# Performance work log

Measured on AMD Instinct MI355X. Metric: run time of the kernel, lower is better.

## Reference

```python
import jax, jax.numpy as jnp
import numpy as np

HQ, HK, D = 16, 4, 64
WINDOW = 1024  # sliding-window left size; right=0 (causal)
GATE_CH = 12
RMS_EPS = 1e-8


def rms_norm(x):
    return x * jax.lax.rsqrt(jnp.mean(x * x, axis=-1, keepdims=True) + RMS_EPS)


def apply_rope(x, cos, sin):
    # x: [B,T,H,D]; cos/sin: [T,D//2] broadcast to [1,T,1,D//2]
    x1, x2 = jnp.split(x, 2, axis=-1)
    c = cos[None, :, None, :]
    s = sin[None, :, None, :]
    return jnp.concatenate([x1 * c - x2 * s, x1 * s + x2 * c], axis=-1)


def setup_inputs() -> dict:
    key = jax.random.key(0)
    ks = jax.random.split(key, 7)
    B, T, E = 2, 2048, HQ * D
    x = jax.random.normal(ks[0], (B, T, E), jnp.float32)
    value_embeds = jax.random.normal(ks[1], (B, T, HK * D), jnp.float32)
    # rope cache: angles for half the head dim
    inv_freq = 1.0 / (10000.0 ** (jnp.arange(D // 2, dtype=jnp.float32) / (D // 2)))
    ang = jnp.arange(T, dtype=jnp.float32)[:, None] * inv_freq[None, :]
    rope_cos = jnp.cos(ang)
    rope_sin = jnp.sin(ang)
    std = (3.0 ** 0.5) * (E ** -0.5)
    w_qkv = jax.random.uniform(ks[2], ((HQ + 2 * HK) * D, E), jnp.float32, -std, std)
    w_gate = jax.random.normal(ks[3], (HK, GATE_CH), jnp.float32) * 0.02
    w_o = jax.random.normal(ks[4], (E, E), jnp.float32) * 0.02
    return {"x": x, "value_embeds": value_embeds, "rope_cos": rope_cos,
            "rope_sin": rope_sin, "w_qkv": w_qkv, "w_gate": w_gate, "w_o": w_o}


def reference(x, value_embeds, rope_cos, rope_sin, w_qkv, w_gate, w_o):
    B, T, E = x.shape
    groups = HQ // HK
    qkv = jnp.einsum('bte,fe->btf', x, w_qkv).reshape(B, T, HQ + 2 * HK, D)
    q = qkv[:, :, :HQ, :]
    k = qkv[:, :, HQ:HQ + HK, :]
    v = qkv[:, :, HQ + HK:, :]
    # value-embedding gating
    ve = value_embeds.reshape(B, T, HK, D)
    gate = 3.0 * jax.nn.sigmoid(jnp.einsum('btc,hc->bth', x[..., :GATE_CH], w_gate))
    v = v + gate[..., None] * ve
    # rope + qk-norm
    q = rms_norm(apply_rope(q, rope_cos, rope_sin))
    k = rms_norm(apply_rope(k, rope_cos, rope_sin))
    # GQA: repeat kv heads
    k_rep = jnp.repeat(k, groups, axis=2)  # [B,T,HQ,D]
    v_rep = jnp.repeat(v, groups, axis=2)
    scale = 1.0 / jnp.sqrt(jnp.float32(D))
    scores = jnp.einsum('bqhd,bkhd->bhqk', q, k_rep) * scale
    i = jnp.arange(T)[:, None]
    j = jnp.arange(T)[None, :]
    mask = (j <= i) & (j >= i - WINDOW)  # causal + sliding window
    scores = jnp.where(mask[None, None], scores, jnp.float32(-1e30))
    attn = jax.nn.softmax(scores, axis=-1)
    out = jnp.einsum('bhqk,bkhd->bqhd', attn, v_rep).reshape(B, T, E)
    out = jnp.einsum('bte,fe->btf', out, w_o)
    return out
```

## Files before the change

kernel.cpp:

```cpp
#include <hip/hip_runtime.h>
#include <math.h>

#define T_LEN 2048
#define NB 2
#define E_DIM 1024
#define F_DIM 1536
#define HQn 16
#define HKn 4
#define Dh 64
#define WIN 1024
#define GATE_CH 12
#define PS 72
#define PSV 68
#define CS 73

typedef unsigned short u16;
typedef unsigned int u32;
typedef __attribute__((ext_vector_type(8))) short bf16x8;
typedef __attribute__((ext_vector_type(4))) short bf16x4;
typedef __attribute__((ext_vector_type(4))) float f32x4;

#if __has_builtin(__builtin_amdgcn_mfma_f32_16x16x16bf16_1k)
#define MFMA16(A, B, C) __builtin_amdgcn_mfma_f32_16x16x16bf16_1k(A, B, C, 0, 0, 0)
#elif __has_builtin(__builtin_amdgcn_mfma_f32_16x16x16_bf16)
#define MFMA16(A, B, C) __builtin_amdgcn_mfma_f32_16x16x16_bf16(A, B, C, 0, 0, 0)
#else
static __device__ __forceinline__ f32x4 mfma16_asm(bf16x4 a, bf16x4 b, f32x4 c) {
  f32x4 d;
  asm volatile("s_nop 1\n\tv_mfma_f32_16x16x16_bf16 %0, %1, %2, %3\n\ts_nop 7\n\ts_nop 7"
               : "=v"(d) : "v"(a), "v"(b), "v"(c));
  return d;
}
#define MFMA16(A, B, C) mfma16_asm(A, B, C)
#endif

__device__ __forceinline__ u16 f2bf(float f) {
  union { float f; unsigned int u; } v; v.f = f;
  unsigned int u = v.u + 0x7FFF + ((v.u >> 16) & 1);
  return (u16)(u >> 16);
}
__device__ __forceinline__ float bf2f(u16 h) {
  union { unsigned int u; float f; } v; v.u = ((unsigned int)h) << 16;
  return v.f;
}
__device__ __forceinline__ u32 pack_bf2(float hi, float lo) {
  union { float f; u32 u; } a, b; a.f = hi; b.f = lo;
  return __builtin_amdgcn_perm(a.u + 0x8000u, b.u + 0x8000u, 0x07060302u);
}
__device__ __forceinline__ void async_copy16(const void* g, void* l) {
  __builtin_amdgcn_global_load_lds(
      (const __attribute__((address_space(1))) unsigned int*)g,
      (__attribute__((address_space(3))) unsigned int*)l, 16, 0, 0);
}

__global__ __launch_bounds__(256) void cvt_all(
    const float4* __restrict__ x, const float4* __restrict__ wqkv,
    const float4* __restrict__ wo, uint2* __restrict__ xb,
    uint2* __restrict__ wqb, uint2* __restrict__ wob)
{
  int blk = blockIdx.x;
  const float4* in; uint2* out; int i;
  if (blk < 4096)       { in = x;    out = xb;  i = blk * 256 + threadIdx.x; }
  else if (blk < 5632)  { in = wqkv; out = wqb; i = (blk - 4096) * 256 + threadIdx.x; }
  else                  { in = wo;   out = wob; i = (blk - 5632) * 256 + threadIdx.x; }
  float4 v = in[i];
  uint2 o;
  o.x = (unsigned)f2bf(v.x) | ((unsigned)f2bf(v.y) << 16);
  o.y = (unsigned)f2bf(v.z) | ((unsigned)f2bf(v.w) << 16);
  out[i] = o;
}

__global__ __launch_bounds__(256) void gemm_qkv(
    const u16* __restrict__ A, const u16* __restrict__ B,
    const float* __restrict__ x, const float* __restrict__ ve,
    const float* __restrict__ rcos, const float* __restrict__ rsin,
    const float* __restrict__ wg,
    u16* __restrict__ qa, u16* __restrict__ ka, u16* __restrict__ vt)
{
  constexpr int K = E_DIM;
  __shared__ u16 smem[8192];
  __shared__ float gateL[64];
  u16* As = smem;
  u16* Bs = smem + 4096;
  u16* Ct = smem;
  const int tid = threadIdx.x;
  const int wave = tid >> 6, lane = tid & 63;
  const int quad = lane >> 4, lanelow = lane & 15;
  const int row0 = blockIdx.x * 64;
  const int h    = blockIdx.y;
  const int col0 = h * 64;
  const int wm = (wave >> 1) * 32, wn = (wave & 1) * 32;

  f32x4 acc[2][2];
#pragma unroll
  for (int i = 0; i < 2; ++i)
#pragma unroll
    for (int j = 0; j < 2; ++j) acc[i][j] = (f32x4){0.f, 0.f, 0.f, 0.f};

  for (int k0 = 0; k0 < K; k0 += 64) {
    __syncthreads();
#pragma unroll
    for (int kk = 0; kk < 2; ++kk) {
      async_copy16(A + (size_t)(row0 + (tid >> 2)) * K + k0 + kk * 32 + (tid & 3) * 8,
                   &As[kk * 2048 + tid * 8]);
      async_copy16(B + (size_t)(col0 + (tid >> 2)) * K + k0 + kk * 32 + (tid & 3) * 8,
                   &Bs[kk * 2048 + tid * 8]);
    }
    __syncthreads();
#pragma unroll
    for (int kk = 0; kk < 2; ++kk) {
      bf16x8 a[2], b[2];
#pragma unroll
      for (int i = 0; i < 2; ++i)
        a[i] = *(const bf16x8*)&As[kk * 2048 + (wm + i * 16 + lanelow) * 32 + quad * 8];
#pragma unroll
      for (int j = 0; j < 2; ++j)
        b[j] = *(const bf16x8*)&Bs[kk * 2048 + (wn + j * 16 + lanelow) * 32 + quad * 8];
#pragma unroll
      for (int i = 0; i < 2; ++i)
#pragma unroll
        for (int j = 0; j < 2; ++j)
          acc[i][j] = __builtin_amdgcn_mfma_f32_16x16x32_bf16(a[i], b[j], acc[i][j], 0, 0, 0);
    }
  }

  __syncthreads();
#pragma unroll
  for (int i = 0; i < 2; ++i)
#pragma unroll
    for (int j = 0; j < 2; ++j)
#pragma unroll
      for (int reg = 0; reg < 4; ++reg) {
        int row = wm + i * 16 + quad * 4 + reg;
        int col = wn + j * 16 + lanelow;
        Ct[row * CS + col] = f2bf(acc[i][j][reg]);
      }
  __syncthreads();

  if (h < HQn + HKn) {
    const bool isq = (h < HQn);
    const int half = lane & 31;
    for (int t = wave * 16; t < wave * 16 + 16; ++t) {
      int tok = row0 + t;
      int tt = tok & (T_LEN - 1);
      float c = rcos[tt * 32 + half], s = rsin[tt * 32 + half];
      float x1 = bf2f(Ct[t * CS + half]);
      float x2 = bf2f(Ct[t * CS + half + 32]);
      float y = (lane < 32) ? (x1 * c - x2 * s) : (x1 * s + x2 * c);
      float ss = y * y;
#pragma unroll
      for (int o = 32; o; o >>= 1) ss += __shfl_xor(ss, o, 64);
      float v = y * rsqrtf(ss * (1.f / Dh) + 1e-8f);
      if (isq)
        qa[((size_t)tok * HQn + h) * Dh + lane] = f2bf(v * 0.1803368801f);
      else
        ka[((size_t)tok * HKn + (h - HQn)) * Dh + lane] = f2bf(v);
    }
  } else {
    const int hk = h - (HQn + HKn);
    if (tid < 64) {
      int tok = row0 + tid;
      float g = 0.f;
#pragma unroll
      for (int c = 0; c < GATE_CH; ++c)
        g += x[(size_t)tok * E_DIM + c] * wg[hk * GATE_CH + c];
      gateL[tid] = 3.f / (1.f + __expf(-g));
    }
    __syncthreads();
    for (int t = wave * 16; t < wave * 16 + 16; ++t) {
      int tok = row0 + t;
      float val = bf2f(Ct[t * CS + lane]) +
                  gateL[t] * ve[(size_t)tok * (HKn * Dh) + hk * Dh + lane];
      Ct[t * CS + lane] = f2bf(val);
    }
    __syncthreads();
    int d = tid >> 2, tseg = (tid & 3) * 16;
    int tokbase = row0 + tseg;
    int b = tokbase >> 11;
    int tloc = tokbase & (T_LEN - 1);
    u16 tmp[16];
#pragma unroll
    for (int e = 0; e < 16; ++e) tmp[e] = Ct[(tseg + e) * CS + d];
    u16* dst = vt + ((size_t)(b * HKn + hk) * Dh + d) * T_LEN + tloc;
#pragma unroll
    for (int p = 0; p < 2; ++p)
      *(uint4*)(dst + p * 8) = *(uint4*)&tmp[p * 8];
  }
}

template<int BM, int BN, int STORE_BF16>
__global__ __launch_bounds__(256) void gemm_async(
    const u16* __restrict__ A, const u16* __restrict__ B,
    void* __restrict__ Cv, int M, int N, int K)
{
  constexpr int MI = BM / 32, NJ = BN / 32;
  constexpr int NSA = BM / 64;
  constexpr int NSB = BN / 64;
  __shared__ u16 As[2][BM * 32];
  __shared__ u16 Bs[2][BN * 32];
  const int tid = threadIdx.x;
  const int wave = tid >> 6, lane = tid & 63;
  const int quad = lane >> 4, lanelow = lane & 15;
  const int row0 = blockIdx.x * BM;
  const int col0 = blockIdx.y * BN;
  const int wm = (wave >> 1) * (BM / 2), wn = (wave & 1) * (BN / 2);

  f32x4 acc[MI][NJ];
#pragma unroll
  for (int i = 0; i < MI; ++i)
#pragma unroll
    for (int j = 0; j < NJ; ++j) acc[i][j] = (f32x4){0.f, 0.f, 0.f, 0.f};

  for (int k0 = 0; k0 < K; k0 += 64) {
    __syncthreads();
#pragma unroll
    for (int kk = 0; kk < 2; ++kk) {
#pragma unroll
      for (int s = 0; s < NSA; ++s) {
        int slot = s * 256 + tid;
        async_copy16(A + (size_t)(row0 + (slot >> 2)) * K + k0 + kk * 32 + (slot & 3) * 8,
                     &As[kk][slot * 8]);
      }
#pragma unroll
      for (int s = 0; s < NSB; ++s) {
        int slot = s * 256 + tid;
        async_copy16(B + (size_t)(col0 + (slot >> 2)) * K + k0 + kk * 32 + (slot & 3) * 8,
                     &Bs[kk][slot * 8]);
      }
    }
    __syncthreads();
#pragma unroll
    for (int kk = 0; kk < 2; ++kk) {
      bf16x8 a[MI], b[NJ];
#pragma unroll
      for (int i = 0; i < MI; ++i)
        a[i] = *(const bf16x8*)&As[kk][(wm + i * 16 + lanelow) * 32 + quad * 8];
#pragma unroll
      for (int j = 0; j < NJ; ++j)
        b[j] = *(const bf16x8*)&Bs[kk][(wn + j * 16 + lanelow) * 32 + quad * 8];
#pragma unroll
      for (int i = 0; i < MI; ++i)
#pragma unroll
        for (int j = 0; j < NJ; ++j)
          acc[i][j] = __builtin_amdgcn_mfma_f32_16x16x32_bf16(a[i], b[j], acc[i][j], 0, 0, 0);
    }
  }

#pragma unroll
  for (int i = 0; i < MI; ++i)
#pragma unroll
    for (int j = 0; j < NJ; ++j) {
      int r = row0 + wm + i * 16 + quad * 4;
      int c = col0 + wn + j * 16 + lanelow;
#pragma unroll
      for (int reg = 0; reg < 4; ++reg) {
        if (STORE_BF16)
          ((u16*)Cv)[(size_t)(r + reg) * N + c] = f2bf(acc[i][j][reg]);
        else
          ((float*)Cv)[(size_t)(r + reg) * N + c] = acc[i][j][reg];
      }
    }
}

__global__ __launch_bounds__(256) void attn_mfma(
    const u16* __restrict__ qa, const u16* __restrict__ ka,
    const u16* __restrict__ vt_g, u16* __restrict__ att)
{
  __shared__ u16 Ks[2][64 * PS];
  __shared__ u16 Vt[2][64 * PSV];
  const int bx = blockIdx.x, h = blockIdx.y, b = blockIdx.z;
  const int j5 = bx & 7;
  const int t5 = (bx >> 3) & 3;
  const int tu = (t5 + (h >> 3) + 2 * b) & 3;
  const int qt = (tu == 0) ? j5
               : (tu == 1) ? (15 - j5)
                           : (16 + 2 * j5 + (tu & 1));
  const int hk = h >> 2;
  const int qb = qt * 64;
  const int tid = threadIdx.x;
  const int wave = tid >> 6, lane = tid & 63;
  const int quad = lane >> 4, lanelow = lane & 15;

  bf16x8 aQ[2];
#pragma unroll
  for (int kk = 0; kk < 2; ++kk)
    aQ[kk] = *(const bf16x8*)(qa +
        ((size_t)(b * T_LEN + qb + wave * 16 + lanelow) * HQn + h) * Dh +
        kk * 32 + quad * 8);

  f32x4 O[4];
  float l = 0.f;
#pragma unroll
  for (int dt = 0; dt < 4; ++dt) O[dt] = (f32x4){0.f, 0.f, 0.f, 0.f};

  const int kt0 = (qt >= 16) ? qt - 16 : 0;
  const int kt1 = qt;

  const int sr0 = tid >> 3,         sc0 = (tid & 7) * 8;
  const int sr1 = (tid + 256) >> 3, sc1 = ((tid + 256) & 7) * 8;
  const u16* kg = ka + (size_t)(b * T_LEN) * (HKn * Dh) + hk * Dh;
  const u16* vg = vt_g + (size_t)(b * HKn + hk) * Dh * T_LEN;

  {
    const int kb = kt0 * 64;
    uint4 k0 = *(const uint4*)(kg + (size_t)(kb + sr0) * (HKn * Dh) + sc0);
    uint4 k1 = *(const uint4*)(kg + (size_t)(kb + sr1) * (HKn * Dh) + sc1);
    uint4 v0 = *(const uint4*)(vg + (size_t)sr0 * T_LEN + kb + sc0);
    uint4 v1 = *(const uint4*)(vg + (size_t)sr1 * T_LEN + kb + sc1);
    *(uint4*)&Ks[0][sr0 * PS + sc0] = k0;
    *(uint4*)&Ks[0][sr1 * PS + sc1] = k1;
    *(uint2*)&Vt[0][sr0 * PSV + sc0]     = make_uint2(v0.x, v0.y);
    *(uint2*)&Vt[0][sr0 * PSV + sc0 + 4] = make_uint2(v0.z, v0.w);
    *(uint2*)&Vt[0][sr1 * PSV + sc1]     = make_uint2(v1.x, v1.y);
    *(uint2*)&Vt[0][sr1 * PSV + sc1 + 4] = make_uint2(v1.z, v1.w);
  }

  for (int kt = kt0; kt <= kt1; ++kt) {
    const int buf = (kt - kt0) & 1;
    const int kb = kt * 64;
    uint4 k0, k1, v0, v1;
    const bool more = (kt < kt1);
    if (more) {
      const int nb = kb + 64;
      k0 = *(const uint4*)(kg + (size_t)(nb + sr0) * (HKn * Dh) + sc0);
      k1 = *(const uint4*)(kg + (size_t)(nb + sr1) * (HKn * Dh) + sc1);
      v0 = *(const uint4*)(vg + (size_t)sr0 * T_LEN + nb + sc0);
      v1 = *(const uint4*)(vg + (size_t)sr1 * T_LEN + nb + sc1);
    }
    __syncthreads();

    f32x4 St[4];
#pragma unroll
    for (int jt = 0; jt < 4; ++jt) {
      bf16x8 aK0 = *(const bf16x8*)&Ks[buf][(jt * 16 + lanelow) * PS + quad * 8];
      bf16x8 aK1 = *(const bf16x8*)&Ks[buf][(jt * 16 + lanelow) * PS + 32 + quad * 8];
      f32x4 acc = (f32x4){-12.f, -12.f, -12.f, -12.f};
      acc = __builtin_amdgcn_mfma_f32_16x16x32_bf16(aK0, aQ[0], acc, 0, 0, 0);
      acc = __builtin_amdgcn_mfma_f32_16x16x32_bf16(aK1, aQ[1], acc, 0, 0, 0);
      St[jt] = acc;
    }
    if (kt == kt1) {
#pragma unroll
      for (int jt = 0; jt < 4; ++jt)
#pragma unroll
        for (int rr = 0; rr < 4; ++rr) {
          int ig = qb + wave * 16 + lanelow;
          int jg = kb + jt * 16 + quad * 4 + rr;
          if (jg > ig) St[jt][rr] = -1e30f;
        }
    } else if (kt == kt0 && qt >= 16) {
#pragma unroll
      for (int jt = 0; jt < 4; ++jt)
#pragma unroll
        for (int rr = 0; rr < 4; ++rr) {
          int ig = qb + wave * 16 + lanelow;
          int jg = kb + jt * 16 + quad * 4 + rr;
          if (jg < ig - WIN) St[jt][rr] = -1e30f;
        }
    }
    bf16x4 Pt[4];
#pragma unroll
    for (int jt = 0; jt < 4; ++jt) {
      float p0 = __builtin_amdgcn_exp2f(St[jt][0]);
      float p1 = __builtin_amdgcn_exp2f(St[jt][1]);
      float p2 = __builtin_amdgcn_exp2f(St[jt][2]);
      float p3 = __builtin_amdgcn_exp2f(St[jt][3]);
      l += (p0 + p1) + (p2 + p3);
      union { uint2 u; bf16x4 v; } pu;
      pu.u.x = pack_bf2(p1, p0);
      pu.u.y = pack_bf2(p3, p2);
      Pt[jt] = pu.v;
    }
#pragma unroll
    for (int dt = 0; dt < 4; ++dt)
#pragma unroll
      for (int jt = 0; jt < 4; ++jt) {
        bf16x4 aV = *(const bf16x4*)&Vt[buf][(dt * 16 + lanelow) * PSV + jt * 16 + quad * 4];
        O[dt] = MFMA16(aV, Pt[jt], O[dt]);
      }
    if (more) {
      const int nbuf = buf ^ 1;
      *(uint4*)&Ks[nbuf][sr0 * PS + sc0] = k0;
      *(uint4*)&Ks[nbuf][sr1 * PS + sc1] = k1;
      *(uint2*)&Vt[nbuf][sr0 * PSV + sc0]     = make_uint2(v0.x, v0.y);
      *(uint2*)&Vt[nbuf][sr0 * PSV + sc0 + 4] = make_uint2(v0.z, v0.w);
      *(uint2*)&Vt[nbuf][sr1 * PSV + sc1]     = make_uint2(v1.x, v1.y);
      *(uint2*)&Vt[nbuf][sr1 * PSV + sc1 + 4] = make_uint2(v1.z, v1.w);
    }
  }

  {
    float s = l;
    s += __shfl_xor(s, 16, 64);
    s += __shfl_xor(s, 32, 64);
    float inv = 1.f / s;
    int qg = qb + wave * 16 + lanelow;
    u16* obase = att + (size_t)(b * T_LEN + qg) * E_DIM + h * Dh;
#pragma unroll
    for (int dt = 0; dt < 4; ++dt) {
      bf16x4 ov;
      ov[0] = (short)f2bf(O[dt][0] * inv);
      ov[1] = (short)f2bf(O[dt][1] * inv);
      ov[2] = (short)f2bf(O[dt][2] * inv);
      ov[3] = (short)f2bf(O[dt][3] * inv);
      *(bf16x4*)(obase + dt * 16 + quad * 4) = ov;
    }
  }
}

extern "C" void kernel_launch(void* const* d_in, const int* in_sizes, int n_in,
                              void* d_out, int out_size, void* d_ws, size_t ws_size,
                              hipStream_t stream)
{
  const float* x    = (const float*)d_in[0];
  const float* ve   = (const float*)d_in[1];
  const float* rc   = (const float*)d_in[2];
  const float* rs   = (const float*)d_in[3];
  const float* wqkv = (const float*)d_in[4];
  const float* wg   = (const float*)d_in[5];
  const float* wo   = (const float*)d_in[6];
  float* out = (float*)d_out;

  char* ws = (char*)d_ws;
  u16* x_bf    = (u16*)(ws);
  u16* wqkv_bf = (u16*)(ws + 8388608);
  u16* wo_bf   = (u16*)(ws + 11534336);
  u16* q_att   = (u16*)(ws + 13631488);
  u16* k_att   = (u16*)(ws + 22020096);
  u16* v_t     = (u16*)(ws + 24117248);
  u16* att     = (u16*)(ws + 26214400);

  cvt_all<<<6656, 256, 0, stream>>>((const float4*)x, (const float4*)wqkv,
                                    (const float4*)wo, (uint2*)x_bf,
                                    (uint2*)wqkv_bf, (uint2*)wo_bf);
  gemm_qkv<<<dim3(64, 24), 256, 0, stream>>>(x_bf, wqkv_bf, x, ve, rc, rs, wg,
                                             q_att, k_att, v_t);
  attn_mfma<<<dim3(T_LEN / 64, HQn, NB), 256, 0, stream>>>(q_att, k_att, v_t, att);
  gemm_async<64, 64, 0><<<dim3(64, 16), 256, 0, stream>>>(
      att, wo_bf, out, 4096, E_DIM, E_DIM);
}
```

Measured before the change: 161.0 us.

## Double-buffer GEMM smem with XOR swizzle and enlarge M tiles to 128

Both GEMM kernels now keep two shared-memory buffers and prefetch the next K tile with async copies while the MFMAs run on the current one, so only one barrier per iteration remains. The shared tiles use a 64-wide row layout with an XOR swizzle to avoid LDS bank conflicts on the fragment reads. The QKV and output GEMMs grow from 64 to 128 rows per block, which improves operand reuse but halves the grid, so occupancy and wave count per CU drop. Shared memory use rises accordingly, and the QKV epilogue loops are resized for the larger tile.

```diff
diff --git a/kernel.cpp b/kernel.cpp
--- a/kernel.cpp
+++ b/kernel.cpp
@@ -78,55 +78,72 @@
     u16* __restrict__ qa, u16* __restrict__ ka, u16* __restrict__ vt)
 {
   constexpr int K = E_DIM;
-  __shared__ u16 smem[8192];
-  __shared__ float gateL[64];
+  __shared__ u16 smem[24576];
+  __shared__ float gateL[128];
   u16* As = smem;
-  u16* Bs = smem + 4096;
+  u16* Bs = smem + 16384;
   u16* Ct = smem;
   const int tid = threadIdx.x;
   const int wave = tid >> 6, lane = tid & 63;
   const int quad = lane >> 4, lanelow = lane & 15;
-  const int row0 = blockIdx.x * 64;
+  const int row0 = blockIdx.x * 128;
   const int h    = blockIdx.y;
   const int col0 = h * 64;
-  const int wm = (wave >> 1) * 32, wn = (wave & 1) * 32;
-
-  f32x4 acc[2][2];
-#pragma unroll
-  for (int i = 0; i < 2; ++i)
+  const int wm = (wave >> 1) * 64, wn = (wave & 1) * 32;
+
+  f32x4 acc[4][2];
+#pragma unroll
+  for (int i = 0; i < 4; ++i)
 #pragma unroll
     for (int j = 0; j < 2; ++j) acc[i][j] = (f32x4){0.f, 0.f, 0.f, 0.f};
 
+  auto stage = [&](int buf, int k0) {
+#pragma unroll
+    for (int s = 0; s < 4; ++s) {
+      int slot = s * 256 + tid;
+      int r = slot >> 3, g = (slot & 7) ^ (r & 7);
+      async_copy16(A + (size_t)(row0 + r) * K + k0 + g * 8,
+                   &As[buf * 8192 + slot * 8]);
+    }
+#pragma unroll
+    for (int s = 0; s < 2; ++s) {
+      int slot = s * 256 + tid;
+      int r = slot >> 3, g = (slot & 7) ^ (r & 7);
+      async_copy16(B + (size_t)(col0 + r) * K + k0 + g * 8,
+                   &Bs[buf * 4096 + slot * 8]);
+    }
+  };
+
+  stage(0, 0);
+  __syncthreads();
+  int cur = 0;
   for (int k0 = 0; k0 < K; k0 += 64) {
-    __syncthreads();
+    if (k0 + 64 < K) stage(cur ^ 1, k0 + 64);
 #pragma unroll
     for (int kk = 0; kk < 2; ++kk) {
-      async_copy16(A + (size_t)(row0 + (tid >> 2)) * K + k0 + kk * 32 + (tid & 3) * 8,
-                   &As[kk * 2048 + tid * 8]);
-      async_copy16(B + (size_t)(col0 + (tid >> 2)) * K + k0 + kk * 32 + (tid & 3) * 8,
-                   &Bs[kk * 2048 + tid * 8]);
-    }
-    __syncthreads();
-#pragma unroll
-    for (int kk = 0; kk < 2; ++kk) {
-      bf16x8 a[2], b[2];
-#pragma unroll
-      for (int i = 0; i < 2; ++i)
-        a[i] = *(const bf16x8*)&As[kk * 2048 + (wm + i * 16 + lanelow) * 32 + quad * 8];
-#pragma unroll
-      for (int j = 0; j < 2; ++j)
-        b[j] = *(const bf16x8*)&Bs[kk * 2048 + (wn + j * 16 + lanelow) * 32 + quad * 8];
-#pragma unroll
-      for (int i = 0; i < 2; ++i)
+      bf16x8 a[4], b[2];
+#pragma unroll
+      for (int i = 0; i < 4; ++i) {
+        int r = wm + i * 16 + lanelow;
+        a[i] = *(const bf16x8*)&As[cur * 8192 + r * 64 + (((kk * 4 + quad) ^ (r & 7)) * 8)];
+      }
+#pragma unroll
+      for (int j = 0; j < 2; ++j) {
+        int r = wn + j * 16 + lanelow;
+        b[j] = *(const bf16x8*)&Bs[cur * 4096 + r * 64 + (((kk * 4 + quad) ^ (r & 7)) * 8)];
+      }
+#pragma unroll
+      for (int i = 0; i < 4; ++i)
 #pragma unroll
         for (int j = 0; j < 2; ++j)
           acc[i][j] = __builtin_amdgcn_mfma_f32_16x16x32_bf16(a[i], b[j], acc[i][j], 0, 0, 0);
     }
-  }
-
-  __syncthreads();
-#pragma unroll
-  for (int i = 0; i < 2; ++i)
+    __syncthreads();
+    cur ^= 1;
+  }
+
+#pragma unroll
+  for (int i = 0; i < 4; ++i)
 #pragma unroll
     for (int j = 0; j < 2; ++j)
 #pragma unroll
@@ -140,7 +157,7 @@
   if (h < HQn + HKn) {
     const bool isq = (h < HQn);
     const int half = lane & 31;
-    for (int t = wave * 16; t < wave * 16 + 16; ++t) {
+    for (int t = wave * 32; t < wave * 32 + 32; ++t) {
       int tok = row0 + t;
       int tt = tok & (T_LEN - 1);
       float c = rcos[tt * 32 + half], s = rsin[tt * 32 + half];
@@ -158,7 +175,7 @@
     }
   } else {
     const int hk = h - (HQn + HKn);
-    if (tid < 64) {
+    if (tid < 128) {
       int tok = row0 + tid;
       float g = 0.f;
 #pragma unroll
@@ -167,23 +184,23 @@
       gateL[tid] = 3.f / (1.f + __expf(-g));
     }
     __syncthreads();
-    for (int t = wave * 16; t < wave * 16 + 16; ++t) {
+    for (int t = wave * 32; t < wave * 32 + 32; ++t) {
       int tok = row0 + t;
       float val = bf2f(Ct[t * CS + lane]) +
                   gateL[t] * ve[(size_t)tok * (HKn * Dh) + hk * Dh + lane];
       Ct[t * CS + lane] = f2bf(val);
     }
     __syncthreads();
-    int d = tid >> 2, tseg = (tid & 3) * 16;
+    int d = tid >> 2, tseg = (tid & 3) * 32;
     int tokbase = row0 + tseg;
     int b = tokbase >> 11;
     int tloc = tokbase & (T_LEN - 1);
-    u16 tmp[16];
-#pragma unroll
-    for (int e = 0; e < 16; ++e) tmp[e] = Ct[(tseg + e) * CS + d];
+    u16 tmp[32];
+#pragma unroll
+    for (int e = 0; e < 32; ++e) tmp[e] = Ct[(tseg + e) * CS + d];
     u16* dst = vt + ((size_t)(b * HKn + hk) * Dh + d) * T_LEN + tloc;
 #pragma unroll
-    for (int p = 0; p < 2; ++p)
+    for (int p = 0; p < 4; ++p)
       *(uint4*)(dst + p * 8) = *(uint4*)&tmp[p * 8];
   }
 }
@@ -194,10 +211,10 @@
     void* __restrict__ Cv, int M, int N, int K)
 {
   constexpr int MI = BM / 32, NJ = BN / 32;
-  constexpr int NSA = BM / 64;
-  constexpr int NSB = BN / 64;
-  __shared__ u16 As[2][BM * 32];
-  __shared__ u16 Bs[2][BN * 32];
+  constexpr int NSA = BM / 32;
+  constexpr int NSB = BN / 32;
+  __shared__ u16 As[2][BM * 64];
+  __shared__ u16 Bs[2][BN * 64];
   const int tid = threadIdx.x;
   const int wave = tid >> 6, lane = tid & 63;
   const int quad = lane >> 4, lanelow = lane & 15;
@@ -211,39 +228,47 @@
 #pragma unroll
     for (int j = 0; j < NJ; ++j) acc[i][j] = (f32x4){0.f, 0.f, 0.f, 0.f};
 
+  auto stage = [&](int buf, int k0) {
+#pragma unroll
+    for (int s = 0; s < NSA; ++s) {
+      int slot = s * 256 + tid;
+      int r = slot >> 3, g = (slot & 7) ^ (r & 7);
+      async_copy16(A + (size_t)(row0 + r) * K + k0 + g * 8, &As[buf][slot * 8]);
+    }
+#pragma unroll
+    for (int s = 0; s < NSB; ++s) {
+      int slot = s * 256 + tid;
+      int r = slot >> 3, g = (slot & 7) ^ (r & 7);
+      async_copy16(B + (size_t)(col0 + r) * K + k0 + g * 8, &Bs[buf][slot * 8]);
+    }
+  };
+
+  stage(0, 0);
+  __syncthreads();
+  int cur = 0;
   for (int k0 = 0; k0 < K; k0 += 64) {
-    __syncthreads();
-#pragma unroll
-    for (int kk = 0; kk < 2; ++kk) {
-#pragma unroll
-      for (int s = 0; s < NSA; ++s) {
-        int slot = s * 256 + tid;
-        async_copy16(A + (size_t)(row0 + (slot >> 2)) * K + k0 + kk * 32 + (slot & 3) * 8,
-                     &As[kk][slot * 8]);
-      }
-#pragma unroll
-      for (int s = 0; s < NSB; ++s) {
-        int slot = s * 256 + tid;
-        async_copy16(B + (size_t)(col0 + (slot >> 2)) * K + k0 + kk * 32 + (slot & 3) * 8,
-                     &Bs[kk][slot * 8]);
-      }
-    }
-    __syncthreads();
+    if (k0 + 64 < K) stage(cur ^ 1, k0 + 64);
 #pragma unroll
     for (int kk = 0; kk < 2; ++kk) {
       bf16x8 a[MI], b[NJ];
 #pragma unroll
-      for (int i = 0; i < MI; ++i)
-        a[i] = *(const bf16x8*)&As[kk][(wm + i * 16 + lanelow) * 32 + quad * 8];
-#pragma unroll
-      for (int j = 0; j < NJ; ++j)
-        b[j] = *(const bf16x8*)&Bs[kk][(wn + j * 16 + lanelow) * 32 + quad * 8];
+      for (int i = 0; i < MI; ++i) {
+        int r = wm + i * 16 + lanelow;
+        a[i] = *(const bf16x8*)&As[cur][r * 64 + (((kk * 4 + quad) ^ (r & 7)) * 8)];
+      }
+#pragma unroll
+      for (int j = 0; j < NJ; ++j) {
+        int r = wn + j * 16 + lanelow;
+        b[j] = *(const bf16x8*)&Bs[cur][r * 64 + (((kk * 4 + quad) ^ (r & 7)) * 8)];
+      }
 #pragma unroll
       for (int i = 0; i < MI; ++i)
 #pragma unroll
         for (int j = 0; j < NJ; ++j)
           acc[i][j] = __builtin_amdgcn_mfma_f32_16x16x32_bf16(a[i], b[j], acc[i][j], 0, 0, 0);
     }
+    __syncthreads();
+    cur ^= 1;
   }
 
 #pragma unroll
@@ -433,9 +458,9 @@
   cvt_all<<<6656, 256, 0, stream>>>((const float4*)x, (const float4*)wqkv,
                                     (const float4*)wo, (uint2*)x_bf,
                                     (uint2*)wqkv_bf, (uint2*)wo_bf);
-  gemm_qkv<<<dim3(64, 24), 256, 0, stream>>>(x_bf, wqkv_bf, x, ve, rc, rs, wg,
+  gemm_qkv<<<dim3(32, 24), 256, 0, stream>>>(x_bf, wqkv_bf, x, ve, rc, rs, wg,
                                              q_att, k_att, v_t);
   attn_mfma<<<dim3(T_LEN / 64, HQn, NB), 256, 0, stream>>>(q_att, k_att, v_t, att);
-  gemm_async<64, 64, 0><<<dim3(64, 16), 256, 0, stream>>>(
+  gemm_async<128, 64, 0><<<dim3(32, 16), 256, 0, stream>>>(
       att, wo_bf, out, 4096, E_DIM, E_DIM);
 }
```

Result: no change. 163.0 us (+1.2%).
